# Kernel optimization log

Hardware: AMD Instinct MI355X
Metric: run time of the kernel (lower is better)

Reference implementation:

```python
import jax, jax.numpy as jnp
import numpy as np

B, H, W, C, N = 4, 64, 2650, 64, 680000
THR = 0.5  # model_cfg.FOREGROUND_THRESHOLD


def setup_inputs() -> dict:
    key = jax.random.key(0)
    k1, k2, k3, k4, k5, k6 = jax.random.split(key, 6)
    pts = jax.random.normal(k1, (N, 5), dtype=jnp.float32)
    bidx = jax.random.randint(k2, (N,), 0, B)
    points = pts.at[:, 0].set(bidx.astype(jnp.float32))  # col 0 = batch index
    ri_h = jax.random.randint(k3, (N, 1), 0, H)
    ri_w = jax.random.randint(k4, (N, 1), 0, W)
    ri_indices = jnp.concatenate([ri_h, ri_w], axis=1).astype(jnp.int32)
    seg_pred = jax.random.uniform(k5, (B, H, W), dtype=jnp.float32)
    range_features = jax.random.normal(k6, (B, C, H, W), dtype=jnp.float32)
    return {"points": points, "ri_indices": ri_indices,
            "seg_pred": seg_pred, "range_features": range_features}


def reference(points, ri_indices, seg_pred, range_features):
    # Fully-vectorized version of the per-batch loop: each point gathers its
    # range-image feature/seg score via a flat (b*H*W + r*W + c) index.
    Bn, Cc, Hh, Ww = range_features.shape
    feats_flat = jnp.transpose(range_features, (0, 2, 3, 1)).reshape(Bn * Hh * Ww, Cc)
    seg_flat = seg_pred.reshape(Bn * Hh * Ww)
    b = points[:, 0].astype(jnp.int32)
    flat_idx = b * (Hh * Ww) + ri_indices[:, 0].astype(jnp.int32) * Ww + ri_indices[:, 1].astype(jnp.int32)  # [N]
    mask = seg_flat[flat_idx] >= THR                    # foreground mask [N] bool
    point_feats = feats_flat[flat_idx]                  # [N, C] gather
    out = jnp.concatenate([points, point_feats], axis=1)  # [N, 5+C]
    # jit-compatible stand-in for boolean compaction: zero out background rows
    out = out * mask[:, None].astype(out.dtype)
    return out, mask
```

## Files before the change

kernel.cpp:

```cpp
#include <hip/hip_runtime.h>

#define B_   4
#define H_   64
#define W_   2650
#define C_   64
#define N_   680000
#define THR_ 0.5f
#define HW_  (H_ * W_)
#define W16_ 166
#define M2_  (B_ * H_ * W16_)
#define NB2_ (M2_ / 256)
#define SPR_ 21
#define NSTRIP_ (B_ * H_ * SPR_)
#define ROWF_ 129
#define NROWBLK_ (N_ / 64)


__global__ void zero_bin_kernel(int* __restrict__ p) {
    p[blockIdx.x * 256 + threadIdx.x] = 0;
}

__global__ __launch_bounds__(256) void bgzero_kernel(
    const float* __restrict__ pts, const int* __restrict__ ri,
    const float* __restrict__ seg,
    float* __restrict__ out, float* __restrict__ mask_out)
{
    __shared__ unsigned long long fgmask_lds;
    const int t    = threadIdx.x;
    const int row0 = blockIdx.x * 64;
    if (t < 64) {
        const int row = row0 + t;
        const int b   = (int)pts[(size_t)row * 5];
        const int2 rc = ((const int2*)ri)[row];
        const bool fg = seg[(size_t)b * HW_ + rc.x * W_ + rc.y] >= THR_;
        const unsigned long long bm = __ballot(fg);
        if (t == 0) fgmask_lds = bm;
        if (!fg) mask_out[row] = 0.0f;
    }
    __syncthreads();
    const unsigned long long m = fgmask_lds;
    const size_t base = (size_t)row0 * 69;
#pragma unroll
    for (int it = 0; it < 18; ++it) {
        const int d = it * 256 + t;
        if (d >= 4416) break;
        const int row = (unsigned)d / 69u;
        if (!((m >> row) & 1ULL)) out[base + d] = 0.0f;
    }
}

__global__ void hist_kernel(const float* __restrict__ pts,
                            const int* __restrict__ ri,
                            const float* __restrict__ seg,
                            int* __restrict__ binarr) {
    int i = blockIdx.x * 256 + threadIdx.x;
    if (i >= N_) return;
    int b = (int)pts[(size_t)i * 5];
    int2 rc = ((const int2*)ri)[i];
    if (seg[(size_t)b * HW_ + rc.x * W_ + rc.y] >= THR_)
        atomicAdd(&binarr[(b * H_ + rc.x) * W16_ + (rc.y >> 4)], 1);
}

__global__ void scan1_kernel(int* __restrict__ binarr, int* __restrict__ bsum) {
    __shared__ int lds[256];
    int t = threadIdx.x;
    int g = blockIdx.x * 256 + t;
    int v = binarr[g];
    lds[t] = v;
    __syncthreads();
    for (int off = 1; off < 256; off <<= 1) {
        int x = (t >= off) ? lds[t - off] : 0;
        __syncthreads();
        lds[t] += x;
        __syncthreads();
    }
    binarr[g] = lds[t] - v;
    if (t == 255) bsum[blockIdx.x] = lds[255];
}

__global__ void scan2_kernel(int* __restrict__ bsum) {
    __shared__ int lds[256];
    int t = threadIdx.x;
    int v = (t < NB2_) ? bsum[t] : 0;
    lds[t] = v;
    __syncthreads();
    for (int off = 1; off < 256; off <<= 1) {
        int x = (t >= off) ? lds[t - off] : 0;
        __syncthreads();
        lds[t] += x;
        __syncthreads();
    }
    if (t < NB2_) bsum[t] = lds[t] - v;
}

__global__ void scan3_kernel(int* __restrict__ binarr, const int* __restrict__ bsum) {
    int g = blockIdx.x * 256 + threadIdx.x;
    binarr[g] += bsum[blockIdx.x];
}

__global__ void scatter_kernel(const float* __restrict__ pts,
                               const int* __restrict__ ri,
                               const float* __restrict__ seg,
                               int* __restrict__ binarr,
                               int* __restrict__ perm) {
    int i = blockIdx.x * 256 + threadIdx.x;
    if (i >= N_) return;
    int b   = (int)pts[(size_t)i * 5];
    int2 rc = ((const int2*)ri)[i];
    int r = rc.x, c = rc.y;
    if (seg[(size_t)b * HW_ + r * W_ + c] < THR_) return;
    int bin  = (b * H_ + r) * W16_ + (c >> 4);
    int slot = atomicAdd(&binarr[bin], 1);
    perm[slot] = i | ((c & 127) << 20);
}

__global__ __launch_bounds__(256) void gather_kernel(
    const float* __restrict__ pts,
    const float* __restrict__ feat,
    const int*   __restrict__ binarr,
    const int*   __restrict__ perm,
    float* __restrict__ out,
    float* __restrict__ mask_out)
{
    __shared__ float flds[64 * ROWF_];
    __shared__ float alds[4][64 * 5];
    const int t    = threadIdx.x;
    const int lane = t & 63;
    const int w    = t >> 6;

    const int sx  = blockIdx.x % SPR_;
    const int tmp = blockIdx.x / SPR_;
    const int r   = tmp & (H_ - 1);
    const int b   = tmp >> 6;

    const int rowbin  = (b * H_ + r) * W16_;
    const int first   = rowbin + sx * 8;
    const int lastbin = rowbin + min(sx * 8 + 8, W16_) - 1;
    const int start   = (first == 0) ? 0 : binarr[first - 1];
    const int end     = binarr[lastbin];
    if (start == end) return;

    const int tot = end - start;
    const int q = tot >> 2, rm = tot & 3;
    const int wstart = start + w * q + min(w, rm);
    const int wend   = wstart + q + (w < rm ? 1 : 0);

    int cnt = min(wend - wstart, 64);
    int rec_l = (lane < cnt) ? perm[wstart + lane] : 0;

    const int c0 = sx * 128;
    if (c0 + 128 <= W_) {
#pragma unroll
        for (int g = 0; g < 16; g++) {
            const int ch = 4 * g + w;
            const int x  = 2 * (lane);
            const float2 v = *(const float2*)(feat + (size_t)(b * C_ + ch) * HW_
                                              + (size_t)r * W_ + c0 + x);
            flds[ch * ROWF_ + x]     = v.x;
            flds[ch * ROWF_ + x + 1] = v.y;
        }
    } else {
#pragma unroll
        for (int g = 0; g < 16; g++) {
            const int ch = 4 * g + w;
            const int x  = 2 * (lane);
            int c1 = c0 + x;     if (c1 >= W_) c1 = W_ - 1;
            int c2 = c0 + x + 1; if (c2 >= W_) c2 = W_ - 1;
            const size_t base = (size_t)(b * C_ + ch) * HW_ + (size_t)r * W_;
            flds[ch * ROWF_ + x]     = feat[base + c1];
            flds[ch * ROWF_ + x + 1] = feat[base + c2];
        }
    }
    __syncthreads();
    if (wstart >= wend) return;

    float* arow = alds[w];
    const float* myrow = &flds[lane * ROWF_];
    int p0 = wstart;
    for (;;) {
        const int na = cnt * 5;
        for (int rbase = 0; rbase < na; rbase += 64) {
            int idx = rbase + lane;
            int pj  = idx / 5;
            int a   = idx - pj * 5;
            int pjc = (idx < na) ? pj : 0;
            int ptj = __shfl(rec_l, pjc) & 0xFFFFF;
            if (idx < na) arow[idx] = pts[(size_t)ptj * 5 + a];
        }
#pragma unroll 4
        for (int j = 0; j < cnt; j++) {
            const int rec = __shfl(rec_l, j);
            const int pt  = rec & 0xFFFFF;
            const float f = myrow[(rec >> 20) & 127];
            const size_t orow = (size_t)pt * 69;
            out[orow + 5 + lane] = f;
            if (lane < 5) out[orow + lane] = arow[j * 5 + lane];
            if (lane == 0) mask_out[pt] = 1.0f;
        }
        p0 += cnt;
        if (p0 >= wend) break;
        cnt = min(wend - p0, 64);
        rec_l = (lane < cnt) ? perm[p0 + lane] : 0;
    }
}

__global__ __launch_bounds__(256) void gather_fallback(
    const float* __restrict__ pts, const int* __restrict__ ri,
    const float* __restrict__ seg, const float* __restrict__ feat,
    float* __restrict__ out, float* __restrict__ mask_out)
{
    const int lane = threadIdx.x & 63;
    const int pt   = blockIdx.x * 4 + (threadIdx.x >> 6);
    if (pt >= N_) return;
    int b = (int)pts[(size_t)pt * 5];
    int r = ri[pt * 2], c = ri[pt * 2 + 1];
    int rc = r * W_ + c;
    float m = (seg[b * HW_ + rc] >= THR_) ? 1.0f : 0.0f;
    float f = feat[(size_t)b * (C_ * HW_) + (size_t)lane * HW_ + rc];
    size_t orow = (size_t)pt * 69;
    out[orow + 5 + lane] = f * m;
    if (lane < 5) out[orow + lane] = pts[(size_t)pt * 5 + lane] * m;
    if (lane == 0) mask_out[pt] = m;
}


extern "C" void kernel_launch(void* const* d_in, const int* in_sizes, int n_in,
                              void* d_out, int out_size, void* d_ws, size_t ws_size,
                              hipStream_t stream) {
    const float* points = (const float*)d_in[0];
    const int*   ri     = (const int*)  d_in[1];
    const float* seg    = (const float*)d_in[2];
    const float* feat   = (const float*)d_in[3];

    float* out      = (float*)d_out;
    float* mask_out = (float*)d_out + (size_t)N_ * 69;

    int* binarr = (int*)d_ws;
    int* bsum   = binarr + M2_;
    int* perm   = bsum + 256;
    const size_t needed = ((size_t)M2_ + 256 + N_) * sizeof(int);
    const bool use_sort = (ws_size >= needed);

    const int nblkN = (N_ + 255) / 256;

    if (use_sort) {
        zero_bin_kernel<<<NB2_,    256, 0, stream>>>(binarr);
        hist_kernel    <<<nblkN,   256, 0, stream>>>(points, ri, seg, binarr);
        scan1_kernel   <<<NB2_,    256, 0, stream>>>(binarr, bsum);
        scan2_kernel   <<<1,       256, 0, stream>>>(bsum);
        scan3_kernel   <<<NB2_,    256, 0, stream>>>(binarr, bsum);
        scatter_kernel <<<nblkN,   256, 0, stream>>>(points, ri, seg, binarr, perm);
        bgzero_kernel  <<<NROWBLK_, 256, 0, stream>>>(points, ri, seg, out, mask_out);
        gather_kernel  <<<NSTRIP_, 256, 0, stream>>>(points, feat, binarr, perm,
                                                     out, mask_out);
    } else {
        gather_fallback<<<(N_ + 3) / 4, 256, 0, stream>>>(points, ri, seg, feat,
                                                          out, mask_out);
    }
}
```

Baseline: 438.7 us.

## Fuse zeroing into histogram, drop scan3, carry point payload through scatter

```diff
diff --git a/kernel.cpp b/kernel.cpp
--- a/kernel.cpp
+++ b/kernel.cpp
@@ -13,52 +13,30 @@
 #define SPR_ 21
 #define NSTRIP_ (B_ * H_ * SPR_)
 #define ROWF_ 129
-#define NROWBLK_ (N_ / 64)
 
 
 __global__ void zero_bin_kernel(int* __restrict__ p) {
     p[blockIdx.x * 256 + threadIdx.x] = 0;
 }
 
-__global__ __launch_bounds__(256) void bgzero_kernel(
+__global__ __launch_bounds__(256) void hist_zero_kernel(
     const float* __restrict__ pts, const int* __restrict__ ri,
     const float* __restrict__ seg,
-    float* __restrict__ out, float* __restrict__ mask_out)
+    int* __restrict__ binarr, float4* __restrict__ outz)
 {
-    __shared__ unsigned long long fgmask_lds;
-    const int t    = threadIdx.x;
-    const int row0 = blockIdx.x * 64;
-    if (t < 64) {
-        const int row = row0 + t;
-        const int b   = (int)pts[(size_t)row * 5];
-        const int2 rc = ((const int2*)ri)[row];
-        const bool fg = seg[(size_t)b * HW_ + rc.x * W_ + rc.y] >= THR_;
-        const unsigned long long bm = __ballot(fg);
-        if (t == 0) fgmask_lds = bm;
-        if (!fg) mask_out[row] = 0.0f;
-    }
-    __syncthreads();
-    const unsigned long long m = fgmask_lds;
-    const size_t base = (size_t)row0 * 69;
-#pragma unroll
-    for (int it = 0; it < 18; ++it) {
-        const int d = it * 256 + t;
-        if (d >= 4416) break;
-        const int row = (unsigned)d / 69u;
-        if (!((m >> row) & 1ULL)) out[base + d] = 0.0f;
-    }
-}
-
-__global__ void hist_kernel(const float* __restrict__ pts,
-                            const int* __restrict__ ri,
-                            const float* __restrict__ seg,
-                            int* __restrict__ binarr) {
-    int i = blockIdx.x * 256 + threadIdx.x;
-    if (i >= N_) return;
-    int b = (int)pts[(size_t)i * 5];
-    int2 rc = ((const int2*)ri)[i];
-    if (seg[(size_t)b * HW_ + rc.x * W_ + rc.y] >= THR_)
-        atomicAdd(&binarr[(b * H_ + rc.x) * W16_ + (rc.y >> 4)], 1);
+    const int i = blockIdx.x * 256 + threadIdx.x;
+    if (i < N_) {
+        int b = (int)pts[(size_t)i * 5];
+        int2 rc = ((const int2*)ri)[i];
+        if (seg[(size_t)b * HW_ + rc.x * W_ + rc.y] >= THR_)
+            atomicAdd(&binarr[(b * H_ + rc.x) * W16_ + (rc.y >> 4)], 1);
+    }
+    const size_t total  = (size_t)N_ * 70 / 4;
+    const size_t stride = (size_t)gridDim.x * 256;
+    const float4 z = {0.f, 0.f, 0.f, 0.f};
+    for (size_t idx = (size_t)blockIdx.x * 256 + threadIdx.x; idx < total;
+         idx += stride)
+        outz[idx] = z;
 }
 
 __global__ void scan1_kernel(int* __restrict__ binarr, int* __restrict__ bsum) {
@@ -93,16 +71,35 @@
     if (t < NB2_) bsum[t] = lds[t] - v;
 }
 
-__global__ void scan3_kernel(int* __restrict__ binarr, const int* __restrict__ bsum) {
-    int g = blockIdx.x * 256 + threadIdx.x;
-    binarr[g] += bsum[blockIdx.x];
-}
-
-__global__ void scatter_kernel(const float* __restrict__ pts,
-                               const int* __restrict__ ri,
-                               const float* __restrict__ seg,
-                               int* __restrict__ binarr,
-                               int* __restrict__ perm) {
+__global__ void scatter_ap_kernel(const float* __restrict__ pts,
+                                  const int* __restrict__ ri,
+                                  const float* __restrict__ seg,
+                                  int* __restrict__ binarr,
+                                  const int* __restrict__ bsum,
+                                  int* __restrict__ aperm) {
+    int i = blockIdx.x * 256 + threadIdx.x;
+    if (i >= N_) return;
+    const float* pr = pts + (size_t)i * 5;
+    float a0 = pr[0], a1 = pr[1], a2 = pr[2], a3 = pr[3], a4 = pr[4];
+    int b = (int)a0;
+    int2 rc = ((const int2*)ri)[i];
+    int r = rc.x, c = rc.y;
+    if (seg[(size_t)b * HW_ + r * W_ + c] < THR_) return;
+    int bin  = (b * H_ + r) * W16_ + (c >> 4);
+    int slot = atomicAdd(&binarr[bin], 1) + bsum[bin >> 8];
+    int rec  = i | ((c & 127) << 20);
+    int2* A2 = (int2*)aperm + (size_t)slot * 3;
+    A2[0] = make_int2(rec, __float_as_int(a0));
+    A2[1] = make_int2(__float_as_int(a1), __float_as_int(a2));
+    A2[2] = make_int2(__float_as_int(a3), __float_as_int(a4));
+}
+
+__global__ void scatter_mid_kernel(const float* __restrict__ pts,
+                                   const int* __restrict__ ri,
+                                   const float* __restrict__ seg,
+                                   int* __restrict__ binarr,
+                                   const int* __restrict__ bsum,
+                                   int* __restrict__ perm) {
     int i = blockIdx.x * 256 + threadIdx.x;
     if (i >= N_) return;
     int b   = (int)pts[(size_t)i * 5];
@@ -110,15 +107,15 @@
     int r = rc.x, c = rc.y;
     if (seg[(size_t)b * HW_ + r * W_ + c] < THR_) return;
     int bin  = (b * H_ + r) * W16_ + (c >> 4);
-    int slot = atomicAdd(&binarr[bin], 1);
+    int slot = atomicAdd(&binarr[bin], 1) + bsum[bin >> 8];
     perm[slot] = i | ((c & 127) << 20);
 }
 
-__global__ __launch_bounds__(256) void gather_kernel(
-    const float* __restrict__ pts,
+__global__ __launch_bounds__(256) void gather_ap_kernel(
     const float* __restrict__ feat,
     const int*   __restrict__ binarr,
-    const int*   __restrict__ perm,
+    const int*   __restrict__ bsum,
+    const int*   __restrict__ aperm,
     float* __restrict__ out,
     float* __restrict__ mask_out)
 {
@@ -136,8 +133,9 @@
     const int rowbin  = (b * H_ + r) * W16_;
     const int first   = rowbin + sx * 8;
     const int lastbin = rowbin + min(sx * 8 + 8, W16_) - 1;
-    const int start   = (first == 0) ? 0 : binarr[first - 1];
-    const int end     = binarr[lastbin];
+    const int start   = (first == 0) ? 0
+                        : binarr[first - 1] + bsum[(first - 1) >> 8];
+    const int end     = binarr[lastbin] + bsum[lastbin >> 8];
     if (start == end) return;
 
     const int tot = end - start;
@@ -145,15 +143,20 @@
     const int wstart = start + w * q + min(w, rm);
     const int wend   = wstart + q + (w < rm ? 1 : 0);
 
+    const int2* A2 = (const int2*)aperm;
     int cnt = min(wend - wstart, 64);
-    int rec_l = (lane < cnt) ? perm[wstart + lane] : 0;
+    int2 q0 = {0, 0}, q1 = {0, 0}, q2 = {0, 0};
+    if (lane < cnt) {
+        size_t rb = (size_t)(wstart + lane) * 3;
+        q0 = A2[rb]; q1 = A2[rb + 1]; q2 = A2[rb + 2];
+    }
 
     const int c0 = sx * 128;
     if (c0 + 128 <= W_) {
 #pragma unroll
         for (int g = 0; g < 16; g++) {
             const int ch = 4 * g + w;
-            const int x  = 2 * (lane);
+            const int x  = 2 * lane;
             const float2 v = *(const float2*)(feat + (size_t)(b * C_ + ch) * HW_
                                               + (size_t)r * W_ + c0 + x);
             flds[ch * ROWF_ + x]     = v.x;
@@ -163,7 +166,101 @@
 #pragma unroll
         for (int g = 0; g < 16; g++) {
             const int ch = 4 * g + w;
-            const int x  = 2 * (lane);
+            const int x  = 2 * lane;
+            int c1 = c0 + x;     if (c1 >= W_) c1 = W_ - 1;
+            int c2 = c0 + x + 1; if (c2 >= W_) c2 = W_ - 1;
+            const size_t base = (size_t)(b * C_ + ch) * HW_ + (size_t)r * W_;
+            flds[ch * ROWF_ + x]     = feat[base + c1];
+            flds[ch * ROWF_ + x + 1] = feat[base + c2];
+        }
+    }
+    __syncthreads();
+    if (wstart >= wend) return;
+
+    float* arow = alds[w];
+    const float* myrow = &flds[lane * ROWF_];
+    int p0 = wstart;
+    for (;;) {
+        if (lane < cnt) {
+            float* d = &arow[lane * 5];
+            d[0] = __int_as_float(q0.y);
+            d[1] = __int_as_float(q1.x);
+            d[2] = __int_as_float(q1.y);
+            d[3] = __int_as_float(q2.x);
+            d[4] = __int_as_float(q2.y);
+        }
+        const int rl0 = q0.x;
+        const int ncnt = min(wend - (p0 + cnt), 64);
+        q0 = make_int2(0, 0); q1 = make_int2(0, 0); q2 = make_int2(0, 0);
+        if (lane < ncnt) {
+            size_t rb = (size_t)(p0 + cnt + lane) * 3;
+            q0 = A2[rb]; q1 = A2[rb + 1]; q2 = A2[rb + 2];
+        }
+#pragma unroll 4
+        for (int j = 0; j < cnt; j++) {
+            const int rec = __shfl(rl0, j);
+            const int pt  = rec & 0xFFFFF;
+            const float f = myrow[(rec >> 20) & 127];
+            const size_t orow = (size_t)pt * 69;
+            out[orow + 5 + lane] = f;
+            if (lane < 5) out[orow + lane] = arow[j * 5 + lane];
+            if (lane == 0) mask_out[pt] = 1.0f;
+        }
+        p0 += cnt;
+        if (p0 >= wend) break;
+        cnt = ncnt;
+    }
+}
+
+__global__ __launch_bounds__(256) void gather_mid_kernel(
+    const float* __restrict__ pts, const float* __restrict__ feat,
+    const int* __restrict__ binarr, const int* __restrict__ bsum,
+    const int* __restrict__ perm,
+    float* __restrict__ out, float* __restrict__ mask_out)
+{
+    __shared__ float flds[64 * ROWF_];
+    __shared__ float alds[4][64 * 5];
+    const int t    = threadIdx.x;
+    const int lane = t & 63;
+    const int w    = t >> 6;
+
+    const int sx  = blockIdx.x % SPR_;
+    const int tmp = blockIdx.x / SPR_;
+    const int r   = tmp & (H_ - 1);
+    const int b   = tmp >> 6;
+
+    const int rowbin  = (b * H_ + r) * W16_;
+    const int first   = rowbin + sx * 8;
+    const int lastbin = rowbin + min(sx * 8 + 8, W16_) - 1;
+    const int start   = (first == 0) ? 0
+                        : binarr[first - 1] + bsum[(first - 1) >> 8];
+    const int end     = binarr[lastbin] + bsum[lastbin >> 8];
+    if (start == end) return;
+
+    const int tot = end - start;
+    const int q = tot >> 2, rm = tot & 3;
+    const int wstart = start + w * q + min(w, rm);
+    const int wend   = wstart + q + (w < rm ? 1 : 0);
+
+    int cnt = min(wend - wstart, 64);
+    int rec_l = (lane < cnt) ? perm[wstart + lane] : 0;
+
+    const int c0 = sx * 128;
+    if (c0 + 128 <= W_) {
+#pragma unroll
+        for (int g = 0; g < 16; g++) {
+            const int ch = 4 * g + w;
+            const int x  = 2 * lane;
+            const float2 v = *(const float2*)(feat + (size_t)(b * C_ + ch) * HW_
+                                              + (size_t)r * W_ + c0 + x);
+            flds[ch * ROWF_ + x]     = v.x;
+            flds[ch * ROWF_ + x + 1] = v.y;
+        }
+    } else {
+#pragma unroll
+        for (int g = 0; g < 16; g++) {
+            const int ch = 4 * g + w;
+            const int x  = 2 * lane;
             int c1 = c0 + x;     if (c1 >= W_) c1 = W_ - 1;
             int c2 = c0 + x + 1; if (c2 >= W_) c2 = W_ - 1;
             const size_t base = (size_t)(b * C_ + ch) * HW_ + (size_t)r * W_;
@@ -237,22 +334,33 @@
 
     int* binarr = (int*)d_ws;
     int* bsum   = binarr + M2_;
-    int* perm   = bsum + 256;
-    const size_t needed = ((size_t)M2_ + 256 + N_) * sizeof(int);
-    const bool use_sort = (ws_size >= needed);
+    int* payload = bsum + 256;
+    const size_t need_ap  = ((size_t)M2_ + 256 + (size_t)N_ * 6) * sizeof(int);
+    const size_t need_mid = ((size_t)M2_ + 256 + N_) * sizeof(int);
 
     const int nblkN = (N_ + 255) / 256;
 
-    if (use_sort) {
-        zero_bin_kernel<<<NB2_,    256, 0, stream>>>(binarr);
-        hist_kernel    <<<nblkN,   256, 0, stream>>>(points, ri, seg, binarr);
-        scan1_kernel   <<<NB2_,    256, 0, stream>>>(binarr, bsum);
-        scan2_kernel   <<<1,       256, 0, stream>>>(bsum);
-        scan3_kernel   <<<NB2_,    256, 0, stream>>>(binarr, bsum);
-        scatter_kernel <<<nblkN,   256, 0, stream>>>(points, ri, seg, binarr, perm);
-        bgzero_kernel  <<<NROWBLK_, 256, 0, stream>>>(points, ri, seg, out, mask_out);
-        gather_kernel  <<<NSTRIP_, 256, 0, stream>>>(points, feat, binarr, perm,
-                                                     out, mask_out);
+    if (ws_size >= need_ap) {
+        zero_bin_kernel<<<NB2_,   256, 0, stream>>>(binarr);
+        hist_zero_kernel<<<nblkN, 256, 0, stream>>>(points, ri, seg, binarr,
+                                                    (float4*)out);
+        scan1_kernel   <<<NB2_,   256, 0, stream>>>(binarr, bsum);
+        scan2_kernel   <<<1,      256, 0, stream>>>(bsum);
+        scatter_ap_kernel<<<nblkN, 256, 0, stream>>>(points, ri, seg, binarr,
+                                                     bsum, payload);
+        gather_ap_kernel<<<NSTRIP_, 256, 0, stream>>>(feat, binarr, bsum,
+                                                      payload, out, mask_out);
+    } else if (ws_size >= need_mid) {
+        zero_bin_kernel<<<NB2_,   256, 0, stream>>>(binarr);
+        hist_zero_kernel<<<nblkN, 256, 0, stream>>>(points, ri, seg, binarr,
+                                                    (float4*)out);
+        scan1_kernel   <<<NB2_,   256, 0, stream>>>(binarr, bsum);
+        scan2_kernel   <<<1,      256, 0, stream>>>(bsum);
+        scatter_mid_kernel<<<nblkN, 256, 0, stream>>>(points, ri, seg, binarr,
+                                                      bsum, payload);
+        gather_mid_kernel<<<NSTRIP_, 256, 0, stream>>>(points, feat, binarr,
+                                                       bsum, payload, out,
+                                                       mask_out);
     } else {
         gather_fallback<<<(N_ + 3) / 4, 256, 0, stream>>>(points, ri, seg, feat,
                                                           out, mask_out);
```

Result: faster. 403.9 us (-7.9%).
